# Optimization experiments

Hardware: AMD Instinct MI355X
Metric: run time of the kernel (lower is better)

## Reference

```python
import jax, jax.numpy as jnp
import numpy as np

NUM_HEADS = 8
MODEL_DIM = 512
HIDDEN_DIM = 64  # model_dim // num_heads
BATCH = 4
SEQ = 1024


def setup_inputs() -> dict:
    key = jax.random.key(0)
    kx, kq, kk, kv, ko = jax.random.split(key, 5)
    # xavier_uniform bound for [model_dim, hidden_dim] fan pair
    bqkv = float(np.sqrt(6.0 / (MODEL_DIM + HIDDEN_DIM)))
    bo = float(np.sqrt(6.0 / (MODEL_DIM + MODEL_DIM)))
    return {
        "X": jax.random.normal(kx, (BATCH, SEQ, MODEL_DIM), dtype=jnp.float32),
        "mask": jnp.zeros((SEQ, SEQ), dtype=bool),  # unused by module
        "Wq": jax.random.uniform(kq, (NUM_HEADS, MODEL_DIM, HIDDEN_DIM), minval=-bqkv, maxval=bqkv, dtype=jnp.float32),
        "Wk": jax.random.uniform(kk, (NUM_HEADS, MODEL_DIM, HIDDEN_DIM), minval=-bqkv, maxval=bqkv, dtype=jnp.float32),
        "Wv": jax.random.uniform(kv, (NUM_HEADS, MODEL_DIM, HIDDEN_DIM), minval=-bqkv, maxval=bqkv, dtype=jnp.float32),
        "Wo": jax.random.uniform(ko, (MODEL_DIM, MODEL_DIM), minval=-bo, maxval=bo, dtype=jnp.float32),
    }


def reference(X, mask, Wq, Wk, Wv, Wo):
    # Per-head projections (replaces the replicated-tensor lin_proj with one einsum)
    q = jnp.einsum("bsm,hmd->hbsd", X, Wq)  # [h,b,s,d]
    k = jnp.einsum("bsm,hmd->hbsd", X, Wk)
    v = jnp.einsum("bsm,hmd->hbsd", X, Wv)
    # Katharopoulos feature map on q and k
    q = jax.nn.elu(q) + 1.0
    k = jax.nn.elu(k) + 1.0
    # Cumulative outer-product state S_t = sum_{i<=t} k_i v_i^T  -> [h,b,s,d,d]
    S = jnp.cumsum(k[..., :, None] * v[..., None, :], axis=2)
    V_bar = jnp.einsum("hbsd,hbsde->hbse", q, S)  # numerator
    Z = jnp.einsum("hbsd,hbsd->hbs", q, jnp.cumsum(k, axis=2))  # normalizer
    out_heads = V_bar / Z[..., None]  # [h,b,s,d]
    # combine_heads: permute to [b,s,h,d], flatten heads, project by Wo
    b, s = out_heads.shape[1], out_heads.shape[2]
    combined = jnp.transpose(out_heads, (1, 2, 0, 3)).reshape(b, s, -1)
    return jnp.einsum("bsm,mn->bsn", combined, Wo)
```

## Files before the change

kernel.cpp:

```cpp
#include <hip/hip_runtime.h>
#include <math.h>

namespace {
typedef unsigned short u16;
typedef __attribute__((ext_vector_type(8))) short bf16x8;
typedef __attribute__((ext_vector_type(4))) float f32x4;

constexpr int H  = 8;
constexpr int B  = 4;
constexpr int S  = 1024;
constexpr int M  = 512;
constexpr int D  = 64;
constexpr int BS = B * S;
constexpr int NC = 16;
constexpr int CH = 64;
constexpr int QSZ = H * B * S * D;
constexpr int NQKV = 3 * M;

__device__ __forceinline__ float elu1(float x) {
  return x > 0.f ? x + 1.f : __expf(x);
}

__device__ __forceinline__ u16 f2bf(float f) {
  unsigned u = __builtin_bit_cast(unsigned, f);
  u += 0x7fffu + ((u >> 16) & 1u);
  return (u16)(u >> 16);
}

__device__ __forceinline__ float bf2f(u16 v) {
  return __builtin_bit_cast(float, ((unsigned)v) << 16);
}

__device__ __forceinline__ void gload16(const u16* g, u16* l) {
  __builtin_amdgcn_global_load_lds(
      (const __attribute__((address_space(1))) unsigned int*)g,
      (__attribute__((address_space(3))) unsigned int*)l, 16, 0, 0);
}

__global__ __launch_bounds__(256) void prep(
    const float* __restrict__ X, const float* __restrict__ Wq,
    const float* __restrict__ Wk, const float* __restrict__ Wv,
    const float* __restrict__ Wo, u16* __restrict__ Xb,
    u16* __restrict__ WCT, u16* __restrict__ WoT) {
  __shared__ float t[64][65];
  const int bid = blockIdx.x;
  if (bid < 2048) {
    const int i = bid * 256 + threadIdx.x;
    const float4 v = reinterpret_cast<const float4*>(X)[i];
    u16 o[4] = {f2bf(v.x), f2bf(v.y), f2bf(v.z), f2bf(v.w)};
    *reinterpret_cast<uint2*>(Xb + i * 4) = *reinterpret_cast<uint2*>(o);
  } else if (bid < 2240) {
    const int bb = bid - 2048;
    const int mt = bb & 7, ph = bb >> 3;
    const int p = ph >> 3, h = ph & 7;
    const float* W = ((p == 0) ? Wq : (p == 1) ? Wk : Wv) + h * (M * D);
    const int m0 = mt * 64;
#pragma unroll
    for (int j = 0; j < 4; ++j) {
      const int i = j * 256 + threadIdx.x;
      const int mm = i >> 4, dd = (i & 15) * 4;
      const float4 v = *reinterpret_cast<const float4*>(W + (m0 + mm) * D + dd);
      t[mm][dd + 0] = v.x; t[mm][dd + 1] = v.y;
      t[mm][dd + 2] = v.z; t[mm][dd + 3] = v.w;
    }
    __syncthreads();
    const int dd = threadIdx.x >> 2, qr = (threadIdx.x & 3) * 16;
    u16* o = WCT + (p * M + h * D + dd) * M + m0 + qr;
#pragma unroll
    for (int i = 0; i < 16; ++i) o[i] = f2bf(t[qr + i][dd]);
  } else {
    const int bb = bid - 2240;
    const int m0 = (bb & 7) * 64, n0 = (bb >> 3) * 64;
#pragma unroll
    for (int j = 0; j < 4; ++j) {
      const int i = j * 256 + threadIdx.x;
      const int mm = i >> 4, nn = (i & 15) * 4;
      const float4 v = *reinterpret_cast<const float4*>(Wo + (m0 + mm) * M + n0 + nn);
      t[mm][nn + 0] = v.x; t[mm][nn + 1] = v.y;
      t[mm][nn + 2] = v.z; t[mm][nn + 3] = v.w;
    }
    __syncthreads();
    const int nn = threadIdx.x >> 2, qr = (threadIdx.x & 3) * 16;
    u16* o = WoT + (n0 + nn) * M + m0 + qr;
#pragma unroll
    for (int i = 0; i < 16; ++i) o[i] = f2bf(t[qr + i][nn]);
  }
}

__global__ __launch_bounds__(256) void gemm_qkv(const u16* __restrict__ A,
                                                const u16* __restrict__ BT,
                                                u16* __restrict__ qb,
                                                u16* __restrict__ kb,
                                                u16* __restrict__ kTb,
                                                u16* __restrict__ vTb) {
  __shared__ alignas(16) u16 As[2][4096];
  __shared__ alignas(16) u16 Bs[2][4096];
  const int tid = threadIdx.x;
  const int wave = tid >> 6, lane = tid & 63;
  const int r0 = blockIdx.x * 128, c0 = blockIdx.y * 128;
  const int wr = (wave >> 1) * 64, wc = (wave & 1) * 64;

  f32x4 acc[4][4] = {};
  const int lrow = tid >> 2;
  const int lk = (tid & 3) * 8;
  const u16* ga0 = A + (size_t)(r0 + lrow) * 512 + lk;
  const u16* ga1 = A + (size_t)(r0 + 64 + lrow) * 512 + lk;
  const u16* gb0 = BT + (size_t)(c0 + lrow) * 512 + lk;
  const u16* gb1 = BT + (size_t)(c0 + 64 + lrow) * 512 + lk;

#define STG_QKV(kt, b)                                \
  {                                                   \
    const int ko = (kt) * 32;                         \
    gload16(ga0 + ko, &As[b][wave * 512]);            \
    gload16(ga1 + ko, &As[b][2048 + wave * 512]);     \
    gload16(gb0 + ko, &Bs[b][wave * 512]);            \
    gload16(gb1 + ko, &Bs[b][2048 + wave * 512]);     \
  }

  STG_QKV(0, 0);
  __syncthreads();
  for (int kt = 0; kt < 16; ++kt) {
    if (kt < 15) STG_QKV(kt + 1, (kt + 1) & 1);
    const bf16x8* As8 = reinterpret_cast<const bf16x8*>(As[kt & 1]);
    const bf16x8* Bs8 = reinterpret_cast<const bf16x8*>(Bs[kt & 1]);
    bf16x8 af[4], bff[4];
#pragma unroll
    for (int mf = 0; mf < 4; ++mf)
      af[mf] = As8[(wr + mf * 16 + (lane & 15)) * 4 + (lane >> 4)];
#pragma unroll
    for (int nf = 0; nf < 4; ++nf)
      bff[nf] = Bs8[(wc + nf * 16 + (lane & 15)) * 4 + (lane >> 4)];
#pragma unroll
    for (int mf = 0; mf < 4; ++mf)
#pragma unroll
      for (int nf = 0; nf < 4; ++nf)
        acc[mf][nf] = __builtin_amdgcn_mfma_f32_16x16x32_bf16(
            af[mf], bff[nf], acc[mf][nf], 0, 0, 0);
    __syncthreads();
  }
#undef STG_QKV

#pragma unroll
  for (int nf = 0; nf < 4; ++nf) {
    const int col = c0 + wc + nf * 16 + (lane & 15);
    const int p = col >> 9, hh = (col >> 6) & 7, dd = col & 63;
#pragma unroll
    for (int mf = 0; mf < 4; ++mf) {
      const int rowb = r0 + wr + mf * 16 + (lane >> 4) * 4;
      const int b = rowb >> 10, s = rowb & 1023;
      const int hb = hh * B + b;
      u16 ov[4];
#pragma unroll
      for (int r = 0; r < 4; ++r) {
        float v = acc[mf][nf][r];
        if (p < 2) v = elu1(v);
        ov[r] = f2bf(v);
      }
      if (p == 0) {
#pragma unroll
        for (int r = 0; r < 4; ++r)
          qb[((size_t)(hb << 10) + s + r) * 64 + dd] = ov[r];
      } else if (p == 1) {
#pragma unroll
        for (int r = 0; r < 4; ++r)
          kb[((size_t)(hb << 10) + s + r) * 64 + dd] = ov[r];
        *reinterpret_cast<uint2*>(kTb + ((size_t)(hb * 64 + dd) << 10) + s) =
            *reinterpret_cast<uint2*>(ov);
      } else {
        *reinterpret_cast<uint2*>(vTb + ((size_t)(hb * 64 + dd) << 10) + s) =
            *reinterpret_cast<uint2*>(ov);
      }
    }
  }
}

__global__ __launch_bounds__(256) void gemm_out(const u16* __restrict__ A,
                                                const u16* __restrict__ BT,
                                                float* __restrict__ out) {
  __shared__ alignas(16) u16 As[2][4096];
  __shared__ alignas(16) u16 Bs[2][2048];
  const int tid = threadIdx.x;
  const int wave = tid >> 6, lane = tid & 63;
  const int r0 = blockIdx.x * 128, c0 = blockIdx.y * 64;
  const int wr = (wave >> 1) * 64, wc = (wave & 1) * 32;

  f32x4 acc[4][2] = {};
  const int lrow = tid >> 2;
  const int lk = (tid & 3) * 8;
  const u16* ga0 = A + (size_t)(r0 + lrow) * 512 + lk;
  const u16* ga1 = A + (size_t)(r0 + 64 + lrow) * 512 + lk;
  const u16* gb0 = BT + (size_t)(c0 + lrow) * 512 + lk;

#define STG_OUT(kt, b)                                \
  {                                                   \
    const int ko = (kt) * 32;                         \
    gload16(ga0 + ko, &As[b][wave * 512]);            \
    gload16(ga1 + ko, &As[b][2048 + wave * 512]);     \
    if (wave < 4) gload16(gb0 + ko, &Bs[b][wave * 512]); \
  }

  STG_OUT(0, 0);
  __syncthreads();
  for (int kt = 0; kt < 16; ++kt) {
    if (kt < 15) STG_OUT(kt + 1, (kt + 1) & 1);
    const bf16x8* As8 = reinterpret_cast<const bf16x8*>(As[kt & 1]);
    const bf16x8* Bs8 = reinterpret_cast<const bf16x8*>(Bs[kt & 1]);
    bf16x8 a[4], b[2];
#pragma unroll
    for (int mf = 0; mf < 4; ++mf)
      a[mf] = As8[(wr + mf * 16 + (lane & 15)) * 4 + (lane >> 4)];
#pragma unroll
    for (int nf = 0; nf < 2; ++nf)
      b[nf] = Bs8[(wc + nf * 16 + (lane & 15)) * 4 + (lane >> 4)];
#pragma unroll
    for (int mf = 0; mf < 4; ++mf)
#pragma unroll
      for (int nf = 0; nf < 2; ++nf)
        acc[mf][nf] = __builtin_amdgcn_mfma_f32_16x16x32_bf16(
            a[mf], b[nf], acc[mf][nf], 0, 0, 0);
    __syncthreads();
  }
#undef STG_OUT

#pragma unroll
  for (int nf = 0; nf < 2; ++nf) {
    const int col = c0 + wc + nf * 16 + (lane & 15);
#pragma unroll
    for (int mf = 0; mf < 4; ++mf)
#pragma unroll
      for (int r = 0; r < 4; ++r) {
        const int row = r0 + wr + mf * 16 + (lane >> 4) * 4 + r;
        out[(size_t)row * M + col] = acc[mf][nf][r];
      }
  }
}

__global__ __launch_bounds__(256) void chunkstate_mfma(
    const u16* __restrict__ kTb, const u16* __restrict__ vTb,
    float* __restrict__ G32, float* __restrict__ Ks) {
  const int tid = threadIdx.x, wave = tid >> 6, lane = tid & 63;
  const int bx = blockIdx.x, hb = bx >> 4, cc = bx & 15, s0 = cc * CH;
  const u16* vbase = vTb + ((size_t)hb * 64) * 1024 + s0;
  const u16* kbase = kTb + ((size_t)hb * 64) * 1024 + s0;

  bf16x8 av[2];
#pragma unroll
  for (int ks = 0; ks < 2; ++ks)
    av[ks] = *reinterpret_cast<const bf16x8*>(
        vbase + (size_t)(wave * 16 + (lane & 15)) * 1024 + ks * 32 + (lane >> 4) * 8);

  f32x4 acc[4] = {};
#pragma unroll
  for (int fd = 0; fd < 4; ++fd)
#pragma unroll
    for (int ks = 0; ks < 2; ++ks) {
      bf16x8 bk = *reinterpret_cast<const bf16x8*>(
          kbase + (size_t)(fd * 16 + (lane & 15)) * 1024 + ks * 32 + (lane >> 4) * 8);
      acc[fd] = __builtin_amdgcn_mfma_f32_16x16x32_bf16(av[ks], bk, acc[fd], 0, 0, 0);
    }

  float* Gp = G32 + (size_t)bx * 4096;
#pragma unroll
  for (int fd = 0; fd < 4; ++fd)
#pragma unroll
    for (int r = 0; r < 4; ++r) {
      const int e = wave * 16 + (lane >> 4) * 4 + r;
      const int d = fd * 16 + (lane & 15);
      Gp[e * 64 + d] = acc[fd][r];
    }

  const int d = tid >> 2, tq = tid & 3;
  const u16* kp = kbase + (size_t)d * 1024 + tq * 16;
  float ks = 0.f;
#pragma unroll
  for (int j = 0; j < 16; ++j) ks += bf2f(kp[j]);
  ks += __shfl_xor(ks, 1);
  ks += __shfl_xor(ks, 2);
  if (tq == 0) Ks[bx * 64 + d] = ks;
}

__global__ __launch_bounds__(256) void prefix_kernel(
    const float* __restrict__ G32, u16* __restrict__ GTb,
    float* __restrict__ Ks) {
  const int hb = blockIdx.x, eg = blockIdx.y;
  const int tid = threadIdx.x;
  const int e = eg * 4 + (tid >> 6), d = tid & 63;
  const size_t base = ((size_t)(hb * 16) * 64 + e) * 64 + d;
  float acc = 0.f;
#pragma unroll
  for (int c = 0; c < 16; ++c) {
    const float v = G32[base + (size_t)c * 4096];
    GTb[base + (size_t)c * 4096] = f2bf(acc);
    acc += v;
  }
  if (eg == 0 && tid < 64) {
    float ka = 0.f;
#pragma unroll
    for (int c = 0; c < 16; ++c) {
      const int idx = (hb * 16 + c) * 64 + tid;
      const float v = Ks[idx];
      Ks[idx] = ka;
      ka += v;
    }
  }
}

__global__ __launch_bounds__(256) void chunkout_mfma(
    const u16* __restrict__ qb, const u16* __restrict__ kb,
    const u16* __restrict__ vTb, const u16* __restrict__ GTb,
    const float* __restrict__ Kc, u16* __restrict__ att) {
  __shared__ alignas(16) u16 Qs[4096], Kls[4096], Vs[4096], Gs[4096], Astg[4096];
  const int tid = threadIdx.x, wave = tid >> 6, lane = tid & 63;
  const int bx = blockIdx.x, hb = bx >> 4, cc = bx & 15, s0 = cc * CH;
  const int h = hb >> 2, b = hb & 3;

  {
    const u16* qg = qb + ((size_t)(hb << 10) + s0) * 64;
    const u16* kg = kb + ((size_t)(hb << 10) + s0) * 64;
    const u16* gg = GTb + (size_t)bx * 4096;
#pragma unroll
    for (int j = 0; j < 2; ++j) {
      const int off = j * 2048 + wave * 512;
      gload16(qg + off + lane * 8, Qs + off);
      gload16(kg + off + lane * 8, Kls + off);
      gload16(gg + off + lane * 8, Gs + off);
    }
    const u16* vg = vTb + ((size_t)hb * 64) * 1024 + s0;
#pragma unroll
    for (int j = 0; j < 2; ++j) {
      const int e0 = j * 32 + wave * 8;
      gload16(vg + (size_t)(e0 + (lane >> 3)) * 1024 + (lane & 7) * 8,
              Vs + e0 * 64);
    }
  }
  __syncthreads();

  const bf16x8* Qs8 = reinterpret_cast<const bf16x8*>(Qs);
  const bf16x8* Ks8 = reinterpret_cast<const bf16x8*>(Kls);
  const bf16x8* Vs8 = reinterpret_cast<const bf16x8*>(Vs);
  const bf16x8* Gs8 = reinterpret_cast<const bf16x8*>(Gs);
  const bf16x8* As8 = reinterpret_cast<const bf16x8*>(Astg);

  const int i0 = wave * 16;
  const int l15 = lane & 15, lk = lane >> 4;

  bf16x8 aq[2];
#pragma unroll
  for (int ks = 0; ks < 2; ++ks)
    aq[ks] = Qs8[(i0 + l15) * 8 + ks * 4 + lk];

  f32x4 a[4] = {};
#pragma unroll
  for (int fj = 0; fj < 4; ++fj)
#pragma unroll
    for (int ks = 0; ks < 2; ++ks) {
      bf16x8 bk = Ks8[(fj * 16 + l15) * 8 + ks * 4 + lk];
      a[fj] = __builtin_amdgcn_mfma_f32_16x16x32_bf16(aq[ks], bk, a[fj], 0, 0, 0);
    }

  const float4 kc4 = *reinterpret_cast<const float4*>(Kc + bx * 64 + l15 * 4);
  float z[4];
  const int rbase = lk * 4;
#pragma unroll
  for (int r = 0; r < 4; ++r) {
    const int il = rbase + r;
    float sum = 0.f;
#pragma unroll
    for (int fj = 0; fj < 4; ++fj) {
      const int j = fj * 16 + l15;
      if (j > i0 + il) a[fj][r] = 0.f;
      sum += a[fj][r];
    }
    const uint2 qrow = *reinterpret_cast<const uint2*>(Qs + (i0 + il) * 64 + l15 * 4);
    const u16* qr16 = reinterpret_cast<const u16*>(&qrow);
    sum += bf2f(qr16[0]) * kc4.x + bf2f(qr16[1]) * kc4.y +
           bf2f(qr16[2]) * kc4.z + bf2f(qr16[3]) * kc4.w;
    z[r] = sum;
  }
#pragma unroll
  for (int off = 1; off <= 8; off <<= 1)
#pragma unroll
    for (int r = 0; r < 4; ++r) z[r] += __shfl_xor(z[r], off);

#pragma unroll
  for (int fj = 0; fj < 4; ++fj)
#pragma unroll
    for (int r = 0; r < 4; ++r)
      Astg[(i0 + rbase + r) * 64 + fj * 16 + l15] = f2bf(a[fj][r]);

  f32x4 o[4] = {};
#pragma unroll
  for (int fe = 0; fe < 4; ++fe) {
#pragma unroll
    for (int ks = 0; ks < 2; ++ks) {
      bf16x8 bg = Gs8[(fe * 16 + l15) * 8 + ks * 4 + lk];
      o[fe] = __builtin_amdgcn_mfma_f32_16x16x32_bf16(aq[ks], bg, o[fe], 0, 0, 0);
    }
#pragma unroll
    for (int ks = 0; ks < 2; ++ks) {
      bf16x8 aa = As8[(i0 + l15) * 8 + ks * 4 + lk];
      bf16x8 bv = Vs8[(fe * 16 + l15) * 8 + ks * 4 + lk];
      o[fe] = __builtin_amdgcn_mfma_f32_16x16x32_bf16(aa, bv, o[fe], 0, 0, 0);
    }
  }

  float rz[4];
#pragma unroll
  for (int r = 0; r < 4; ++r) rz[r] = 1.f / z[r];
#pragma unroll
  for (int fe = 0; fe < 4; ++fe)
#pragma unroll
    for (int r = 0; r < 4; ++r) {
      const int srow = s0 + i0 + rbase + r;
      att[((size_t)(b << 10) + srow) * 512 + h * 64 + fe * 16 + l15] =
          f2bf(o[fe][r] * rz[r]);
    }
}

}

extern "C" void kernel_launch(void* const* d_in, const int* in_sizes, int n_in,
                              void* d_out, int out_size, void* d_ws,
                              size_t ws_size, hipStream_t stream) {
  const float* X  = (const float*)d_in[0];
  const float* Wq = (const float*)d_in[2];
  const float* Wk = (const float*)d_in[3];
  const float* Wv = (const float*)d_in[4];
  const float* Wo = (const float*)d_in[5];
  float* out = (float*)d_out;

  u16* Xb  = (u16*)d_ws;
  u16* att = Xb;
  u16* WCT = Xb + QSZ;
  u16* WoT = WCT + NQKV * M;
  u16* qb  = WoT + M * M;
  u16* kb  = qb + QSZ;
  u16* kTb = kb + QSZ;
  u16* vTb = kTb + QSZ;
  u16* GTb = vTb + QSZ;
  float* G32 = (float*)(GTb + QSZ);
  float* Ks  = G32 + QSZ;

  prep<<<dim3(2304), 256, 0, stream>>>(X, Wq, Wk, Wv, Wo, Xb, WCT, WoT);
  gemm_qkv<<<dim3(BS / 128, NQKV / 128), 256, 0, stream>>>(Xb, WCT, qb, kb,
                                                           kTb, vTb);
  chunkstate_mfma<<<dim3(H * B * NC), 256, 0, stream>>>(kTb, vTb, G32, Ks);
  prefix_kernel<<<dim3(H * B, 16), 256, 0, stream>>>(G32, GTb, Ks);
  chunkout_mfma<<<dim3(H * B * NC), 256, 0, stream>>>(qb, kb, vTb, GTb, Ks,
                                                      att);
  gemm_out<<<dim3(BS / 128, M / 64), 256, 0, stream>>>(att, WoT, out);
}
```

Baseline: 52.63 us.

## Fuse chunk-state, prefix scan and chunk-output kernels into one cooperative kernel

Merges the three middle kernels (per-chunk KV state, cross-chunk prefix scan, chunk output) into a single cooperative launch of 512 blocks, with grid-wide syncs between the phases. This removes two kernel launches and the gaps between them. In exchange it pays for two grid barriers and needs all 512 blocks resident at once, which depends on the LDS use (40KB per block) and the launch bounds of two blocks per CU. If co-residency fails, the cooperative launch errors out.

```diff
diff --git a/kernel.cpp b/kernel.cpp
--- a/kernel.cpp
+++ b/kernel.cpp
@@ -1,5 +1,8 @@
 #include <hip/hip_runtime.h>
+#include <hip/hip_cooperative_groups.h>
 #include <math.h>
+
+namespace cg = cooperative_groups;
 
 namespace {
 typedef unsigned short u16;
@@ -235,186 +238,190 @@
   }
 }
 
-__global__ __launch_bounds__(256) void chunkstate_mfma(
+__global__ __launch_bounds__(256, 2) void middle_fused(
+    const u16* __restrict__ qb, const u16* __restrict__ kb,
     const u16* __restrict__ kTb, const u16* __restrict__ vTb,
-    float* __restrict__ G32, float* __restrict__ Ks) {
-  const int tid = threadIdx.x, wave = tid >> 6, lane = tid & 63;
-  const int bx = blockIdx.x, hb = bx >> 4, cc = bx & 15, s0 = cc * CH;
-  const u16* vbase = vTb + ((size_t)hb * 64) * 1024 + s0;
-  const u16* kbase = kTb + ((size_t)hb * 64) * 1024 + s0;
-
-  bf16x8 av[2];
-#pragma unroll
-  for (int ks = 0; ks < 2; ++ks)
-    av[ks] = *reinterpret_cast<const bf16x8*>(
-        vbase + (size_t)(wave * 16 + (lane & 15)) * 1024 + ks * 32 + (lane >> 4) * 8);
-
-  f32x4 acc[4] = {};
-#pragma unroll
-  for (int fd = 0; fd < 4; ++fd)
-#pragma unroll
-    for (int ks = 0; ks < 2; ++ks) {
-      bf16x8 bk = *reinterpret_cast<const bf16x8*>(
-          kbase + (size_t)(fd * 16 + (lane & 15)) * 1024 + ks * 32 + (lane >> 4) * 8);
-      acc[fd] = __builtin_amdgcn_mfma_f32_16x16x32_bf16(av[ks], bk, acc[fd], 0, 0, 0);
-    }
-
-  float* Gp = G32 + (size_t)bx * 4096;
-#pragma unroll
-  for (int fd = 0; fd < 4; ++fd)
-#pragma unroll
-    for (int r = 0; r < 4; ++r) {
-      const int e = wave * 16 + (lane >> 4) * 4 + r;
-      const int d = fd * 16 + (lane & 15);
-      Gp[e * 64 + d] = acc[fd][r];
-    }
-
-  const int d = tid >> 2, tq = tid & 3;
-  const u16* kp = kbase + (size_t)d * 1024 + tq * 16;
-  float ks = 0.f;
-#pragma unroll
-  for (int j = 0; j < 16; ++j) ks += bf2f(kp[j]);
-  ks += __shfl_xor(ks, 1);
-  ks += __shfl_xor(ks, 2);
-  if (tq == 0) Ks[bx * 64 + d] = ks;
-}
-
-__global__ __launch_bounds__(256) void prefix_kernel(
-    const float* __restrict__ G32, u16* __restrict__ GTb,
-    float* __restrict__ Ks) {
-  const int hb = blockIdx.x, eg = blockIdx.y;
-  const int tid = threadIdx.x;
-  const int e = eg * 4 + (tid >> 6), d = tid & 63;
-  const size_t base = ((size_t)(hb * 16) * 64 + e) * 64 + d;
-  float acc = 0.f;
-#pragma unroll
-  for (int c = 0; c < 16; ++c) {
-    const float v = G32[base + (size_t)c * 4096];
-    GTb[base + (size_t)c * 4096] = f2bf(acc);
-    acc += v;
-  }
-  if (eg == 0 && tid < 64) {
-    float ka = 0.f;
-#pragma unroll
-    for (int c = 0; c < 16; ++c) {
-      const int idx = (hb * 16 + c) * 64 + tid;
-      const float v = Ks[idx];
-      Ks[idx] = ka;
-      ka += v;
-    }
-  }
-}
-
-__global__ __launch_bounds__(256) void chunkout_mfma(
-    const u16* __restrict__ qb, const u16* __restrict__ kb,
-    const u16* __restrict__ vTb, const u16* __restrict__ GTb,
-    const float* __restrict__ Kc, u16* __restrict__ att) {
+    float* __restrict__ G32, float* __restrict__ Ks,
+    u16* __restrict__ GTb, u16* __restrict__ att) {
   __shared__ alignas(16) u16 Qs[4096], Kls[4096], Vs[4096], Gs[4096], Astg[4096];
   const int tid = threadIdx.x, wave = tid >> 6, lane = tid & 63;
-  const int bx = blockIdx.x, hb = bx >> 4, cc = bx & 15, s0 = cc * CH;
-  const int h = hb >> 2, b = hb & 3;
+  const int bxg = blockIdx.x;
+  cg::grid_group grid = cg::this_grid();
 
   {
-    const u16* qg = qb + ((size_t)(hb << 10) + s0) * 64;
-    const u16* kg = kb + ((size_t)(hb << 10) + s0) * 64;
-    const u16* gg = GTb + (size_t)bx * 4096;
-#pragma unroll
-    for (int j = 0; j < 2; ++j) {
-      const int off = j * 2048 + wave * 512;
-      gload16(qg + off + lane * 8, Qs + off);
-      gload16(kg + off + lane * 8, Kls + off);
-      gload16(gg + off + lane * 8, Gs + off);
-    }
-    const u16* vg = vTb + ((size_t)hb * 64) * 1024 + s0;
-#pragma unroll
-    for (int j = 0; j < 2; ++j) {
-      const int e0 = j * 32 + wave * 8;
-      gload16(vg + (size_t)(e0 + (lane >> 3)) * 1024 + (lane & 7) * 8,
-              Vs + e0 * 64);
-    }
-  }
-  __syncthreads();
-
-  const bf16x8* Qs8 = reinterpret_cast<const bf16x8*>(Qs);
-  const bf16x8* Ks8 = reinterpret_cast<const bf16x8*>(Kls);
-  const bf16x8* Vs8 = reinterpret_cast<const bf16x8*>(Vs);
-  const bf16x8* Gs8 = reinterpret_cast<const bf16x8*>(Gs);
-  const bf16x8* As8 = reinterpret_cast<const bf16x8*>(Astg);
-
-  const int i0 = wave * 16;
-  const int l15 = lane & 15, lk = lane >> 4;
-
-  bf16x8 aq[2];
-#pragma unroll
-  for (int ks = 0; ks < 2; ++ks)
-    aq[ks] = Qs8[(i0 + l15) * 8 + ks * 4 + lk];
-
-  f32x4 a[4] = {};
-#pragma unroll
-  for (int fj = 0; fj < 4; ++fj)
-#pragma unroll
-    for (int ks = 0; ks < 2; ++ks) {
-      bf16x8 bk = Ks8[(fj * 16 + l15) * 8 + ks * 4 + lk];
-      a[fj] = __builtin_amdgcn_mfma_f32_16x16x32_bf16(aq[ks], bk, a[fj], 0, 0, 0);
-    }
-
-  const float4 kc4 = *reinterpret_cast<const float4*>(Kc + bx * 64 + l15 * 4);
-  float z[4];
-  const int rbase = lk * 4;
-#pragma unroll
-  for (int r = 0; r < 4; ++r) {
-    const int il = rbase + r;
-    float sum = 0.f;
-#pragma unroll
-    for (int fj = 0; fj < 4; ++fj) {
-      const int j = fj * 16 + l15;
-      if (j > i0 + il) a[fj][r] = 0.f;
-      sum += a[fj][r];
-    }
-    const uint2 qrow = *reinterpret_cast<const uint2*>(Qs + (i0 + il) * 64 + l15 * 4);
-    const u16* qr16 = reinterpret_cast<const u16*>(&qrow);
-    sum += bf2f(qr16[0]) * kc4.x + bf2f(qr16[1]) * kc4.y +
-           bf2f(qr16[2]) * kc4.z + bf2f(qr16[3]) * kc4.w;
-    z[r] = sum;
-  }
-#pragma unroll
-  for (int off = 1; off <= 8; off <<= 1)
-#pragma unroll
-    for (int r = 0; r < 4; ++r) z[r] += __shfl_xor(z[r], off);
-
-#pragma unroll
-  for (int fj = 0; fj < 4; ++fj)
-#pragma unroll
-    for (int r = 0; r < 4; ++r)
-      Astg[(i0 + rbase + r) * 64 + fj * 16 + l15] = f2bf(a[fj][r]);
-
-  f32x4 o[4] = {};
-#pragma unroll
-  for (int fe = 0; fe < 4; ++fe) {
-#pragma unroll
-    for (int ks = 0; ks < 2; ++ks) {
-      bf16x8 bg = Gs8[(fe * 16 + l15) * 8 + ks * 4 + lk];
-      o[fe] = __builtin_amdgcn_mfma_f32_16x16x32_bf16(aq[ks], bg, o[fe], 0, 0, 0);
-    }
-#pragma unroll
-    for (int ks = 0; ks < 2; ++ks) {
-      bf16x8 aa = As8[(i0 + l15) * 8 + ks * 4 + lk];
-      bf16x8 bv = Vs8[(fe * 16 + l15) * 8 + ks * 4 + lk];
-      o[fe] = __builtin_amdgcn_mfma_f32_16x16x32_bf16(aa, bv, o[fe], 0, 0, 0);
-    }
-  }
-
-  float rz[4];
-#pragma unroll
-  for (int r = 0; r < 4; ++r) rz[r] = 1.f / z[r];
-#pragma unroll
-  for (int fe = 0; fe < 4; ++fe)
+    const int bx = bxg, hb = bx >> 4, cc = bx & 15, s0 = cc * CH;
+    const u16* vbase = vTb + ((size_t)hb * 64) * 1024 + s0;
+    const u16* kbase = kTb + ((size_t)hb * 64) * 1024 + s0;
+
+    bf16x8 av[2];
+#pragma unroll
+    for (int ks = 0; ks < 2; ++ks)
+      av[ks] = *reinterpret_cast<const bf16x8*>(
+          vbase + (size_t)(wave * 16 + (lane & 15)) * 1024 + ks * 32 + (lane >> 4) * 8);
+
+    f32x4 acc[4] = {};
+#pragma unroll
+    for (int fd = 0; fd < 4; ++fd)
+#pragma unroll
+      for (int ks = 0; ks < 2; ++ks) {
+        bf16x8 bk = *reinterpret_cast<const bf16x8*>(
+            kbase + (size_t)(fd * 16 + (lane & 15)) * 1024 + ks * 32 + (lane >> 4) * 8);
+        acc[fd] = __builtin_amdgcn_mfma_f32_16x16x32_bf16(av[ks], bk, acc[fd], 0, 0, 0);
+      }
+
+    float* Gp = G32 + (size_t)bx * 4096;
+#pragma unroll
+    for (int fd = 0; fd < 4; ++fd)
+#pragma unroll
+      for (int r = 0; r < 4; ++r) {
+        const int e = wave * 16 + (lane >> 4) * 4 + r;
+        const int d = fd * 16 + (lane & 15);
+        Gp[e * 64 + d] = acc[fd][r];
+      }
+
+    const int d = tid >> 2, tq = tid & 3;
+    const u16* kp = kbase + (size_t)d * 1024 + tq * 16;
+    float ks = 0.f;
+#pragma unroll
+    for (int j = 0; j < 16; ++j) ks += bf2f(kp[j]);
+    ks += __shfl_xor(ks, 1);
+    ks += __shfl_xor(ks, 2);
+    if (tq == 0) Ks[bx * 64 + d] = ks;
+  }
+
+  grid.sync();
+
+  {
+    const int hb = bxg >> 4, eg = bxg & 15;
+    const int e = eg * 4 + (tid >> 6), d = tid & 63;
+    const size_t base = ((size_t)(hb * 16) * 64 + e) * 64 + d;
+    float acc = 0.f;
+#pragma unroll
+    for (int c = 0; c < 16; ++c) {
+      const float v = G32[base + (size_t)c * 4096];
+      GTb[base + (size_t)c * 4096] = f2bf(acc);
+      acc += v;
+    }
+    if (eg == 0 && tid < 64) {
+      float ka = 0.f;
+#pragma unroll
+      for (int c = 0; c < 16; ++c) {
+        const int idx = (hb * 16 + c) * 64 + tid;
+        const float v = Ks[idx];
+        Ks[idx] = ka;
+        ka += v;
+      }
+    }
+  }
+
+  grid.sync();
+
+  {
+    const int bx = bxg, hb = bx >> 4, cc = bx & 15, s0 = cc * CH;
+    const int h = hb >> 2, b = hb & 3;
+
+    {
+      const u16* qg = qb + ((size_t)(hb << 10) + s0) * 64;
+      const u16* kg = kb + ((size_t)(hb << 10) + s0) * 64;
+      const u16* gg = GTb + (size_t)bx * 4096;
+#pragma unroll
+      for (int j = 0; j < 2; ++j) {
+        const int off = j * 2048 + wave * 512;
+        gload16(qg + off + lane * 8, Qs + off);
+        gload16(kg + off + lane * 8, Kls + off);
+        gload16(gg + off + lane * 8, Gs + off);
+      }
+      const u16* vg = vTb + ((size_t)hb * 64) * 1024 + s0;
+#pragma unroll
+      for (int j = 0; j < 2; ++j) {
+        const int e0 = j * 32 + wave * 8;
+        gload16(vg + (size_t)(e0 + (lane >> 3)) * 1024 + (lane & 7) * 8,
+                Vs + e0 * 64);
+      }
+    }
+    __syncthreads();
+
+    const bf16x8* Qs8 = reinterpret_cast<const bf16x8*>(Qs);
+    const bf16x8* Ks8 = reinterpret_cast<const bf16x8*>(Kls);
+    const bf16x8* Vs8 = reinterpret_cast<const bf16x8*>(Vs);
+    const bf16x8* Gs8 = reinterpret_cast<const bf16x8*>(Gs);
+    const bf16x8* As8 = reinterpret_cast<const bf16x8*>(Astg);
+
+    const int i0 = wave * 16;
+    const int l15 = lane & 15, lk = lane >> 4;
+
+    bf16x8 aq[2];
+#pragma unroll
+    for (int ks = 0; ks < 2; ++ks)
+      aq[ks] = Qs8[(i0 + l15) * 8 + ks * 4 + lk];
+
+    f32x4 a[4] = {};
+#pragma unroll
+    for (int fj = 0; fj < 4; ++fj)
+#pragma unroll
+      for (int ks = 0; ks < 2; ++ks) {
+        bf16x8 bk = Ks8[(fj * 16 + l15) * 8 + ks * 4 + lk];
+        a[fj] = __builtin_amdgcn_mfma_f32_16x16x32_bf16(aq[ks], bk, a[fj], 0, 0, 0);
+      }
+
+    const float4 kc4 = *reinterpret_cast<const float4*>(Ks + bx * 64 + l15 * 4);
+    float z[4];
+    const int rbase = lk * 4;
 #pragma unroll
     for (int r = 0; r < 4; ++r) {
-      const int srow = s0 + i0 + rbase + r;
-      att[((size_t)(b << 10) + srow) * 512 + h * 64 + fe * 16 + l15] =
-          f2bf(o[fe][r] * rz[r]);
-    }
+      const int il = rbase + r;
+      float sum = 0.f;
+#pragma unroll
+      for (int fj = 0; fj < 4; ++fj) {
+        const int j = fj * 16 + l15;
+        if (j > i0 + il) a[fj][r] = 0.f;
+        sum += a[fj][r];
+      }
+      const uint2 qrow = *reinterpret_cast<const uint2*>(Qs + (i0 + il) * 64 + l15 * 4);
+      const u16* qr16 = reinterpret_cast<const u16*>(&qrow);
+      sum += bf2f(qr16[0]) * kc4.x + bf2f(qr16[1]) * kc4.y +
+             bf2f(qr16[2]) * kc4.z + bf2f(qr16[3]) * kc4.w;
+      z[r] = sum;
+    }
+#pragma unroll
+    for (int off = 1; off <= 8; off <<= 1)
+#pragma unroll
+      for (int r = 0; r < 4; ++r) z[r] += __shfl_xor(z[r], off);
+
+#pragma unroll
+    for (int fj = 0; fj < 4; ++fj)
+#pragma unroll
+      for (int r = 0; r < 4; ++r)
+        Astg[(i0 + rbase + r) * 64 + fj * 16 + l15] = f2bf(a[fj][r]);
+
+    f32x4 o[4] = {};
+#pragma unroll
+    for (int fe = 0; fe < 4; ++fe) {
+#pragma unroll
+      for (int ks = 0; ks < 2; ++ks) {
+        bf16x8 bg = Gs8[(fe * 16 + l15) * 8 + ks * 4 + lk];
+        o[fe] = __builtin_amdgcn_mfma_f32_16x16x32_bf16(aq[ks], bg, o[fe], 0, 0, 0);
+      }
+#pragma unroll
+      for (int ks = 0; ks < 2; ++ks) {
+        bf16x8 aa = As8[(i0 + l15) * 8 + ks * 4 + lk];
+        bf16x8 bv = Vs8[(fe * 16 + l15) * 8 + ks * 4 + lk];
+        o[fe] = __builtin_amdgcn_mfma_f32_16x16x32_bf16(aa, bv, o[fe], 0, 0, 0);
+      }
+    }
+
+    float rz[4];
+#pragma unroll
+    for (int r = 0; r < 4; ++r) rz[r] = 1.f / z[r];
+#pragma unroll
+    for (int fe = 0; fe < 4; ++fe)
+#pragma unroll
+      for (int r = 0; r < 4; ++r) {
+        const int srow = s0 + i0 + rbase + r;
+        att[((size_t)(b << 10) + srow) * 512 + h * 64 + fe * 16 + l15] =
+            f2bf(o[fe][r] * rz[r]);
+      }
+  }
 }
 
 }
@@ -444,9 +451,11 @@
   prep<<<dim3(2304), 256, 0, stream>>>(X, Wq, Wk, Wv, Wo, Xb, WCT, WoT);
   gemm_qkv<<<dim3(BS / 128, NQKV / 128), 256, 0, stream>>>(Xb, WCT, qb, kb,
                                                            kTb, vTb);
-  chunkstate_mfma<<<dim3(H * B * NC), 256, 0, stream>>>(kTb, vTb, G32, Ks);
-  prefix_kernel<<<dim3(H * B, 16), 256, 0, stream>>>(G32, GTb, Ks);
-  chunkout_mfma<<<dim3(H * B * NC), 256, 0, stream>>>(qb, kb, vTb, GTb, Ks,
-                                                      att);
+  {
+    void* args[] = {(void*)&qb, (void*)&kb, (void*)&kTb, (void*)&vTb,
+                    (void*)&G32, (void*)&Ks, (void*)&GTb, (void*)&att};
+    hipLaunchCooperativeKernel((const void*)middle_fused, dim3(H * B * NC),
+                               dim3(256), args, 0, stream);
+  }
   gemm_out<<<dim3(BS / 128, M / 64), 256, 0, stream>>>(att, WoT, out);
 }
```

Result: slower. 163.9 us (+211.3%).
